# Optimization experiments

Measured on AMD Instinct MI355X. Metric: run time of the kernel, lower is better.

## Reference

```python
import jax, jax.numpy as jnp
import numpy as np

B, N, D = 2, 8192, 1024
H, DH = 8, 64  # heads, dim_head; inner = H*DH = 512
INNER = H * DH


def setup_inputs() -> dict:
    key = jax.random.key(0)
    k1, k2, k3 = jax.random.split(key, 3)
    x = jax.random.normal(k1, (B, N, D), dtype=jnp.float32)
    # xavier_uniform-ish scaling for weights
    W_qkv = jax.random.normal(k2, (D, 3 * INNER), dtype=jnp.float32) * (1.0 / np.sqrt(D))
    W_out = jax.random.normal(k3, (INNER, D), dtype=jnp.float32) * (1.0 / np.sqrt(INNER))
    b_out = jnp.zeros((D,), dtype=jnp.float32)
    return {"x": x, "W_qkv": W_qkv, "W_out": W_out, "b_out": b_out}


def reference(x, W_qkv, W_out, b_out):
    b, n, d = x.shape
    qkv = x @ W_qkv                               # [b, n, 3*inner]
    q, k, v = jnp.split(qkv, 3, axis=-1)          # each [b, n, inner]

    def to_heads(t):
        return t.reshape(b, n, H, DH).transpose(0, 2, 1, 3)  # [b, h, n, dh]

    q, k, v = to_heads(q), to_heads(k), to_heads(v)
    q = jax.nn.softmax(q, axis=-1)                # over dim_head
    k = jax.nn.softmax(k, axis=-2)                # over sequence
    # context: k^T v  -> [b, h, dh, dh]
    context = jnp.einsum('bhnd,bhne->bhde', k, v)
    out = jnp.einsum('bhnd,bhde->bhne', q, context)  # [b, h, n, dh]
    out = out.transpose(0, 2, 1, 3).reshape(b, n, INNER)
    return out @ W_out + b_out                    # [b, n, d]
```

## Files before the change

### kernel.cpp

```cpp
#include <hip/hip_runtime.h>
#include <stdint.h>


typedef _Float16 half4 __attribute__((ext_vector_type(4)));
typedef _Float16 half8 __attribute__((ext_vector_type(8)));
typedef float f32x4 __attribute__((ext_vector_type(4)));

#define WS_XB 0UL
#define WS_WQKVT 33554432UL
#define WS_CWT 37748736UL
#define WS_CTXPART 54525952UL
#define WS_COLPART 71303168UL
#define WS_SQ 88080384UL

__device__ __forceinline__ void gld16(const void* g, void* l) {
  __builtin_amdgcn_global_load_lds(
      (const __attribute__((address_space(1))) unsigned int*)g,
      (__attribute__((address_space(3))) unsigned int*)l, 16, 0, 0);
}

__global__ void prep_kernel(const float* __restrict__ x,
                            const float* __restrict__ Wqkv,
                            _Float16* __restrict__ xb,
                            _Float16* __restrict__ wqkvT) {
  const int blk = blockIdx.x;
  const int t = threadIdx.x;
  if (blk < 16384) {
    int i = blk * 256 + t;
    f32x4 v = *(const f32x4*)(x + (size_t)i * 4);
    half4 h = {(_Float16)v[0], (_Float16)v[1], (_Float16)v[2], (_Float16)v[3]};
    *(half4*)(xb + (size_t)i * 4) = h;
  } else {
    __shared__ float sT[64 * 65];
    const int tb = blk - 16384;
    const int r0 = (tb & 15) * 64, c0 = (tb >> 4) * 64;
    const int lr = t >> 4, lc4 = (t & 15) * 4;
#pragma unroll
    for (int s = 0; s < 4; ++s) {
      const int row = s * 16 + lr;
      f32x4 v = *(const f32x4*)&Wqkv[(size_t)(r0 + row) * 1536 + c0 + lc4];
#pragma unroll
      for (int j = 0; j < 4; ++j) sT[(lc4 + j) * 65 + row] = v[j];
    }
    __syncthreads();
#pragma unroll
    for (int s = 0; s < 4; ++s) {
      const int cl = s * 16 + lr;
      half4 o = {(_Float16)sT[cl * 65 + lc4], (_Float16)sT[cl * 65 + lc4 + 1],
                 (_Float16)sT[cl * 65 + lc4 + 2],
                 (_Float16)sT[cl * 65 + lc4 + 3]};
      *(half4*)&wqkvT[(size_t)(c0 + cl) * 1024 + r0 + lc4] = o;
    }
  }
}


__device__ __forceinline__ void stage_tile(const _Float16* __restrict__ G, int K,
                                           int rowbase, int kt, char* region,
                                           int t) {
  char* wbase = region + (t & ~63) * 16;
#pragma unroll
  for (int q = 0; q < 4; ++q) {
    const int row = q * 32 + (t >> 3);
    const int col8 = ((t & 7) ^ (row & 7)) * 8;
    gld16(G + (size_t)(rowbase + row) * K + kt + col8, wbase + q * 4096);
  }
}

__device__ __forceinline__ void stage_tile64(const _Float16* __restrict__ G,
                                             int K, int rowbase, int kt,
                                             char* region, int t) {
  char* wbase = region + (t & ~63) * 16;
#pragma unroll
  for (int q = 0; q < 2; ++q) {
    const int row = q * 32 + (t >> 3);
    const int col8 = ((t & 7) ^ (row & 7)) * 8;
    gld16(G + (size_t)(rowbase + row) * K + kt + col8, wbase + q * 4096);
  }
}

template <int EPI>
__global__ __launch_bounds__(256, 2) void gemm128(
    const _Float16* __restrict__ A, const _Float16* __restrict__ BT, int K,
    int NTN, int bstride, _Float16* __restrict__ oQ,
    _Float16* __restrict__ ctxpart, float* __restrict__ colpart,
    float* __restrict__ oC, const float* __restrict__ bias) {
  __shared__ char lds[65536];
  const int t = threadIdx.x;
  const int l = t & 63, w = t >> 6;
  const int wm = w >> 1, wn = w & 1;
  const int fr = l & 15, qq = l >> 4;
  const int swzx = (fr & 7) << 4;

  const int nwg = gridDim.x;
  const int cpx = nwg >> 3;
  const int wg = (blockIdx.x & 7) * cpx + (blockIdx.x >> 3);
  const int tileM = wg / NTN, tileN = wg - tileM * NTN;
  const int mbase = tileM * 128, nbase = tileN * 128;
  BT += (size_t)(tileM >> 6) * bstride;

  const int NT = K >> 6;
  f32x4 acc[4][4] = {};
  half8 a[4][2], b[4][2];

  auto STG = [&](int tile) {
    int kt = tile * 64;
    if (kt > K - 64) kt = K - 64;
    char* base = lds + ((tile & 1) << 15);
    stage_tile(A, K, mbase, kt, base, t);
    if (EPI == 1 || tileN < 4) {
      stage_tile(BT, K, nbase, kt, base + 16384, t);
    } else {
      const int h = tileN - 4;
      stage_tile64(BT, K, 512 + h * 64, kt, base + 16384, t);
      stage_tile64(BT, K, 1024 + h * 64, kt, base + 16384 + 8192, t);
    }
  };

  STG(0);
  STG(1);
  asm volatile("s_waitcnt vmcnt(8)" ::: "memory");
  __builtin_amdgcn_s_barrier();

  for (int t2 = 0; t2 < NT; ++t2) {
    const char* ldsA = lds + ((t2 & 1) << 15);
    const char* ldsB = ldsA + 16384;
    STG(t2 + 1);
#pragma unroll
    for (int mi = 0; mi < 4; ++mi)
#pragma unroll
      for (int kk = 0; kk < 2; ++kk) {
        int off = (wm * 64 + mi * 16 + fr) * 128 + ((kk * 64 + qq * 16) ^ swzx);
        a[mi][kk] = *(const half8*)(ldsA + off);
      }
#pragma unroll
    for (int ni = 0; ni < 4; ++ni)
#pragma unroll
      for (int kk = 0; kk < 2; ++kk) {
        int off = (wn * 64 + ni * 16 + fr) * 128 + ((kk * 64 + qq * 16) ^ swzx);
        b[ni][kk] = *(const half8*)(ldsB + off);
      }
    __builtin_amdgcn_s_barrier();
    __builtin_amdgcn_s_setprio(1);
#pragma unroll
    for (int mi = 0; mi < 4; ++mi)
#pragma unroll
      for (int ni = 0; ni < 2; ++ni)
#pragma unroll
        for (int kk = 0; kk < 2; ++kk)
          acc[mi][ni] = __builtin_amdgcn_mfma_f32_16x16x32_f16(
              a[mi][kk], b[ni][kk], acc[mi][ni], 0, 0, 0);
    __builtin_amdgcn_s_setprio(0);
    asm volatile("s_waitcnt vmcnt(0) lgkmcnt(0)" ::: "memory");
    __builtin_amdgcn_s_barrier();
    __builtin_amdgcn_s_setprio(1);
#pragma unroll
    for (int mi = 0; mi < 4; ++mi)
#pragma unroll
      for (int ni = 2; ni < 4; ++ni)
#pragma unroll
        for (int kk = 0; kk < 2; ++kk)
          acc[mi][ni] = __builtin_amdgcn_mfma_f32_16x16x32_f16(
              a[mi][kk], b[ni][kk], acc[mi][ni], 0, 0, 0);
    __builtin_amdgcn_s_setprio(0);
  }

  if (EPI == 0) {
    if (tileN < 4) {
      const int gcol0 = nbase + wn * 64;
#pragma unroll
      for (int mi = 0; mi < 4; ++mi) {
        const int grow = mbase + wm * 64 + mi * 16 + qq * 4;
        float e[4][4], rs[4];
#pragma unroll
        for (int r = 0; r < 4; ++r) {
          float s = 0.f;
#pragma unroll
          for (int ni = 0; ni < 4; ++ni) {
            e[ni][r] = __expf(acc[mi][ni][r]);
            s += e[ni][r];
          }
#pragma unroll
          for (int off = 1; off < 16; off <<= 1) s += __shfl_xor(s, off, 64);
          rs[r] = 1.f / s;
        }
#pragma unroll
        for (int ni = 0; ni < 4; ++ni) {
          const int gcol = gcol0 + ni * 16 + fr;
#pragma unroll
          for (int r = 0; r < 4; ++r)
            oQ[(size_t)(grow + r) * 512 + gcol] = (_Float16)(e[ni][r] * rs[r]);
        }
      }
    } else {
      const int h = tileN - 4;
      float* credu = (float*)(lds + 32768);
      if (wn == 0) {
#pragma unroll
        for (int mi = 0; mi < 4; ++mi)
#pragma unroll
          for (int ni = 0; ni < 4; ++ni) {
            f32x4 e4;
#pragma unroll
            for (int r = 0; r < 4; ++r) e4[r] = __expf(acc[mi][ni][r]);
            acc[mi][ni] = e4;
          }
        float s[4] = {};
#pragma unroll
        for (int ni = 0; ni < 4; ++ni) {
#pragma unroll
          for (int mi = 0; mi < 4; ++mi)
#pragma unroll
            for (int r = 0; r < 4; ++r) s[ni] += acc[mi][ni][r];
          s[ni] += __shfl_xor(s[ni], 16, 64);
          s[ni] += __shfl_xor(s[ni], 32, 64);
        }
        if (l < 16) {
#pragma unroll
          for (int ni = 0; ni < 4; ++ni) credu[wm * 64 + ni * 16 + fr] = s[ni];
        }
      }
      {
        char* dst8 = lds + (wn ? 16384 : 0);
#pragma unroll
        for (int mi = 0; mi < 4; ++mi) {
          const int nb = (wm * 64 + mi * 16 + qq * 4) * 2;
#pragma unroll
          for (int ni = 0; ni < 4; ++ni) {
            const int c = ni * 16 + fr;
            half4 pk = {(_Float16)acc[mi][ni][0], (_Float16)acc[mi][ni][1],
                        (_Float16)acc[mi][ni][2], (_Float16)acc[mi][ni][3]};
            *(half4*)(dst8 + c * 256 + (nb ^ ((c & 15) << 4))) = pk;
          }
        }
      }
      __syncthreads();
      half8 bf[4];
      const int erow = w * 16 + fr;
#pragma unroll
      for (int kk = 0; kk < 4; ++kk)
        bf[kk] = *(const half8*)(lds + 16384 + erow * 256 +
                                 ((kk * 64 + qq * 16) ^ ((erow & 15) << 4)));
      f32x4 dacc[4] = {};
#pragma unroll
      for (int mi = 0; mi < 4; ++mi) {
        const int drow = mi * 16 + fr;
#pragma unroll
        for (int kk = 0; kk < 4; ++kk) {
          half8 af = *(const half8*)(lds + drow * 256 +
                                     ((kk * 64 + qq * 16) ^ ((drow & 15) << 4)));
          dacc[mi] =
              __builtin_amdgcn_mfma_f32_16x16x32_f16(af, bf[kk], dacc[mi], 0, 0, 0);
        }
      }
      const int bh = (tileM >> 6) * 8 + h, chunk = tileM & 63;
      _Float16* cp = ctxpart + ((size_t)bh * 64 + chunk) * 4096;
#pragma unroll
      for (int mi = 0; mi < 4; ++mi)
#pragma unroll
        for (int r = 0; r < 4; ++r)
          cp[(mi * 16 + qq * 4 + r) * 64 + w * 16 + fr] =
              (_Float16)dacc[mi][r];
      if (t < 16) {
        f32x4 c0 = *(const f32x4*)&credu[t * 4];
        f32x4 c1 = *(const f32x4*)&credu[64 + t * 4];
        *(f32x4*)&colpart[((size_t)bh * 64 + chunk) * 64 + t * 4] = c0 + c1;
      }
    }
  } else {
#pragma unroll
    for (int mi = 0; mi < 4; ++mi) {
      const int grow = mbase + wm * 64 + mi * 16 + qq * 4;
#pragma unroll
      for (int ni = 0; ni < 4; ++ni) {
        const int gcol = nbase + wn * 64 + ni * 16 + fr;
        const float bb = bias[gcol];
#pragma unroll
        for (int r = 0; r < 4; ++r)
          oC[(size_t)(grow + r) * 1024 + gcol] = acc[mi][ni][r] + bb;
      }
    }
  }
}

__global__ __launch_bounds__(256) void ctxw_kernel(
    const _Float16* __restrict__ ctxpart, const float* __restrict__ colpart,
    const float* __restrict__ Wout, _Float16* __restrict__ cwT) {
  __shared__ float part[4][64];
  __shared__ float csp[64];
  __shared__ float crow[64];
  const int blk = blockIdx.x;
  const int bh = blk >> 6, d = blk & 63;
  const int b = bh >> 3, h = bh & 7;
  const int t = threadIdx.x;
  const int e = t & 63, cq = t >> 6;
  float p = 0.f;
#pragma unroll
  for (int cc = 0; cc < 16; ++cc)
    p += (float)ctxpart[((size_t)bh * 64 + cq * 16 + cc) * 4096 + d * 64 + e];
  part[cq][e] = p;
  if (t >= 64 && t < 128)
    csp[t - 64] = colpart[((size_t)bh * 64 + (t - 64)) * 64 + d];
  __syncthreads();
  if (t < 64) {
    float csum = 0.f;
#pragma unroll
    for (int c = 0; c < 64; ++c) csum += csp[c];
    crow[t] = (part[0][t] + part[1][t] + part[2][t] + part[3][t]) / csum;
  }
  __syncthreads();
  float acc[4] = {};
  for (int e2 = 0; e2 < 64; ++e2) {
    const float c = crow[e2];
    const float* wr = Wout + (size_t)(h * 64 + e2) * 1024 + t;
#pragma unroll
    for (int j = 0; j < 4; ++j) acc[j] += c * wr[j * 256];
  }
  _Float16* dst = cwT + (size_t)b * 524288 + (size_t)t * 512 + h * 64 + d;
#pragma unroll
  for (int j = 0; j < 4; ++j) dst[(size_t)j * 256 * 512] = (_Float16)acc[j];
}

extern "C" void kernel_launch(void* const* d_in, const int* in_sizes, int n_in,
                              void* d_out, int out_size, void* d_ws, size_t ws_size,
                              hipStream_t stream) {
  const float* x = (const float*)d_in[0];
  const float* Wqkv = (const float*)d_in[1];
  const float* Wout = (const float*)d_in[2];
  const float* bout = (const float*)d_in[3];
  float* out = (float*)d_out;
  char* ws = (char*)d_ws;

  _Float16* xb = (_Float16*)(ws + WS_XB);
  _Float16* wqkvT = (_Float16*)(ws + WS_WQKVT);
  _Float16* cwT = (_Float16*)(ws + WS_CWT);
  _Float16* sq = (_Float16*)(ws + WS_SQ);
  _Float16* ctxpart = (_Float16*)(ws + WS_CTXPART);
  float* colpart = (float*)(ws + WS_COLPART);

  prep_kernel<<<16768, 256, 0, stream>>>(x, Wqkv, xb, wqkvT);
  gemm128<0><<<1536, 256, 0, stream>>>(xb, wqkvT, 1024, 12, 0, sq, ctxpart,
                                       colpart, nullptr, nullptr);
  ctxw_kernel<<<1024, 256, 0, stream>>>(ctxpart, colpart, Wout, cwT);
  gemm128<1><<<1024, 256, 0, stream>>>(sq, cwT, 512, 8, 524288, nullptr,
                                       nullptr, nullptr, out, bout);
}
```

Measured before the change: 131.2 us.

## Switch GEMM mainloop to K=32 tiles with triple-buffered LDS pipeline

The GEMM k-step shrinks from 64 to 32, and a 3-stage LDS ring buffer replaces the double buffer, staging tile t+2 while computing tile t. LDS per block drops from 64KB to 48KB, and launch bounds rise to 3 blocks per CU to improve occupancy and latency hiding. The swizzle pattern is reworked for 64-byte rows. In exchange there are twice as many loop iterations and barriers per K, and the wait counts must exactly match the number of outstanding loads.

```diff
diff --git a/kernel.cpp b/kernel.cpp
--- a/kernel.cpp
+++ b/kernel.cpp
@@ -55,42 +55,38 @@
 }
 
 
-__device__ __forceinline__ void stage_tile(const _Float16* __restrict__ G, int K,
-                                           int rowbase, int kt, char* region,
-                                           int t) {
-  char* wbase = region + (t & ~63) * 16;
-#pragma unroll
-  for (int q = 0; q < 4; ++q) {
-    const int row = q * 32 + (t >> 3);
-    const int col8 = ((t & 7) ^ (row & 7)) * 8;
-    gld16(G + (size_t)(rowbase + row) * K + kt + col8, wbase + q * 4096);
-  }
-}
-
-__device__ __forceinline__ void stage_tile64(const _Float16* __restrict__ G,
-                                             int K, int rowbase, int kt,
-                                             char* region, int t) {
-  char* wbase = region + (t & ~63) * 16;
-#pragma unroll
-  for (int q = 0; q < 2; ++q) {
-    const int row = q * 32 + (t >> 3);
-    const int col8 = ((t & 7) ^ (row & 7)) * 8;
-    gld16(G + (size_t)(rowbase + row) * K + kt + col8, wbase + q * 4096);
-  }
+__device__ __forceinline__ void stage32_128(const _Float16* __restrict__ G,
+                                            int K, int rowbase, int kt,
+                                            char* region, int t) {
+#pragma unroll
+  for (int s = 0; s < 2; ++s) {
+    const int row = s * 64 + (t >> 2);
+    const int srcc = ((t & 3) ^ ((row >> 1) & 3)) * 8;
+    gld16(G + (size_t)(rowbase + row) * K + kt + srcc,
+          region + s * 4096 + (t & ~63) * 16);
+  }
+}
+
+__device__ __forceinline__ void stage32_64(const _Float16* __restrict__ G,
+                                           int K, int rowbase, int kt,
+                                           char* region, int t) {
+  const int row = t >> 2;
+  const int srcc = ((t & 3) ^ ((row >> 1) & 3)) * 8;
+  gld16(G + (size_t)(rowbase + row) * K + kt + srcc, region + (t & ~63) * 16);
 }
 
 template <int EPI>
-__global__ __launch_bounds__(256, 2) void gemm128(
+__global__ __launch_bounds__(256, 3) void gemm128(
     const _Float16* __restrict__ A, const _Float16* __restrict__ BT, int K,
     int NTN, int bstride, _Float16* __restrict__ oQ,
     _Float16* __restrict__ ctxpart, float* __restrict__ colpart,
     float* __restrict__ oC, const float* __restrict__ bias) {
-  __shared__ char lds[65536];
+  __shared__ char lds[49152];
   const int t = threadIdx.x;
   const int l = t & 63, w = t >> 6;
   const int wm = w >> 1, wn = w & 1;
   const int fr = l & 15, qq = l >> 4;
-  const int swzx = (fr & 7) << 4;
+  const int cswz = ((qq ^ ((fr >> 1) & 3)) * 16);
 
   const int nwg = gridDim.x;
   const int cpx = nwg >> 3;
@@ -99,71 +95,61 @@
   const int mbase = tileM * 128, nbase = tileN * 128;
   BT += (size_t)(tileM >> 6) * bstride;
 
-  const int NT = K >> 6;
+  const int NT = K >> 5;
   f32x4 acc[4][4] = {};
-  half8 a[4][2], b[4][2];
+  half8 a[4], b[4];
 
   auto STG = [&](int tile) {
-    int kt = tile * 64;
-    if (kt > K - 64) kt = K - 64;
-    char* base = lds + ((tile & 1) << 15);
-    stage_tile(A, K, mbase, kt, base, t);
+    int kt = tile * 32;
+    if (kt > K - 32) kt = K - 32;
+    char* base = lds + (tile % 3) * 16384;
+    stage32_128(A, K, mbase, kt, base, t);
     if (EPI == 1 || tileN < 4) {
-      stage_tile(BT, K, nbase, kt, base + 16384, t);
+      stage32_128(BT, K, nbase, kt, base + 8192, t);
     } else {
       const int h = tileN - 4;
-      stage_tile64(BT, K, 512 + h * 64, kt, base + 16384, t);
-      stage_tile64(BT, K, 1024 + h * 64, kt, base + 16384 + 8192, t);
+      stage32_64(BT, K, 512 + h * 64, kt, base + 8192, t);
+      stage32_64(BT, K, 1024 + h * 64, kt, base + 8192 + 4096, t);
     }
   };
 
   STG(0);
   STG(1);
-  asm volatile("s_waitcnt vmcnt(8)" ::: "memory");
+  asm volatile("s_waitcnt vmcnt(4)" ::: "memory");
   __builtin_amdgcn_s_barrier();
 
   for (int t2 = 0; t2 < NT; ++t2) {
-    const char* ldsA = lds + ((t2 & 1) << 15);
-    const char* ldsB = ldsA + 16384;
-    STG(t2 + 1);
+    const char* bufc = lds + (t2 % 3) * 16384;
+    const char* ldsA = bufc;
+    const char* ldsB = bufc + 8192;
+    STG(t2 + 2);
 #pragma unroll
     for (int mi = 0; mi < 4; ++mi)
-#pragma unroll
-      for (int kk = 0; kk < 2; ++kk) {
-        int off = (wm * 64 + mi * 16 + fr) * 128 + ((kk * 64 + qq * 16) ^ swzx);
-        a[mi][kk] = *(const half8*)(ldsA + off);
-      }
+      a[mi] = *(const half8*)(ldsA + (wm * 64 + mi * 16 + fr) * 64 + cswz);
 #pragma unroll
     for (int ni = 0; ni < 4; ++ni)
-#pragma unroll
-      for (int kk = 0; kk < 2; ++kk) {
-        int off = (wn * 64 + ni * 16 + fr) * 128 + ((kk * 64 + qq * 16) ^ swzx);
-        b[ni][kk] = *(const half8*)(ldsB + off);
-      }
+      b[ni] = *(const half8*)(ldsB + (wn * 64 + ni * 16 + fr) * 64 + cswz);
+    __builtin_amdgcn_s_setprio(1);
+#pragma unroll
+    for (int mi = 0; mi < 4; ++mi)
+#pragma unroll
+      for (int ni = 0; ni < 2; ++ni)
+        acc[mi][ni] = __builtin_amdgcn_mfma_f32_16x16x32_f16(
+            a[mi], b[ni], acc[mi][ni], 0, 0, 0);
+    __builtin_amdgcn_s_setprio(0);
+    asm volatile("s_waitcnt vmcnt(4) lgkmcnt(0)" ::: "memory");
     __builtin_amdgcn_s_barrier();
     __builtin_amdgcn_s_setprio(1);
 #pragma unroll
     for (int mi = 0; mi < 4; ++mi)
 #pragma unroll
-      for (int ni = 0; ni < 2; ++ni)
-#pragma unroll
-        for (int kk = 0; kk < 2; ++kk)
-          acc[mi][ni] = __builtin_amdgcn_mfma_f32_16x16x32_f16(
-              a[mi][kk], b[ni][kk], acc[mi][ni], 0, 0, 0);
+      for (int ni = 2; ni < 4; ++ni)
+        acc[mi][ni] = __builtin_amdgcn_mfma_f32_16x16x32_f16(
+            a[mi], b[ni], acc[mi][ni], 0, 0, 0);
     __builtin_amdgcn_s_setprio(0);
-    asm volatile("s_waitcnt vmcnt(0) lgkmcnt(0)" ::: "memory");
-    __builtin_amdgcn_s_barrier();
-    __builtin_amdgcn_s_setprio(1);
-#pragma unroll
-    for (int mi = 0; mi < 4; ++mi)
-#pragma unroll
-      for (int ni = 2; ni < 4; ++ni)
-#pragma unroll
-        for (int kk = 0; kk < 2; ++kk)
-          acc[mi][ni] = __builtin_amdgcn_mfma_f32_16x16x32_f16(
-              a[mi][kk], b[ni][kk], acc[mi][ni], 0, 0, 0);
-    __builtin_amdgcn_s_setprio(0);
-  }
+  }
+  asm volatile("s_waitcnt vmcnt(0)" ::: "memory");
+  __builtin_amdgcn_s_barrier();
 
   if (EPI == 0) {
     if (tileN < 4) {
```

Result: slower. 135.9 us (+3.6%).
